# Optimization experiments

Measured on AMD Instinct MI355X. Metric: run time of the kernel, lower is better.

Reference implementation:

```python
import jax, jax.numpy as jnp
import numpy as np

EMBED_DIM = 1024
NUM_HEADS = 16
HEAD_DIM = EMBED_DIM // NUM_HEADS
B, S = 2, 2048


def setup_inputs() -> dict:
    key = jax.random.key(0)
    ks = jax.random.split(key, 10)
    inp = {
        "query": jax.random.normal(ks[0], (B, S, EMBED_DIM), dtype=jnp.float32),
        "key": jax.random.normal(ks[1], (B, S, EMBED_DIM), dtype=jnp.float32),
        "value": jax.random.normal(ks[2], (B, S, EMBED_DIM), dtype=jnp.float32),
        # 0 => masked key position (matches attn_mask == 0 in the torch code)
        "attn_mask": jax.random.randint(ks[3], (B, S), 0, 2, dtype=jnp.int32),
        "Wq": jax.random.normal(ks[4], (EMBED_DIM, EMBED_DIM), dtype=jnp.float32) * 0.02,
        "bq": jnp.zeros((EMBED_DIM,), dtype=jnp.float32),
        "Wk": jax.random.normal(ks[5], (EMBED_DIM, EMBED_DIM), dtype=jnp.float32) * 0.02,
        "bk": jnp.zeros((EMBED_DIM,), dtype=jnp.float32),
        "Wv": jax.random.normal(ks[6], (EMBED_DIM, EMBED_DIM), dtype=jnp.float32) * 0.02,
        "bv": jnp.zeros((EMBED_DIM,), dtype=jnp.float32),
    }
    return inp


def _proj_heads(x, W, b):
    # x: [B, S, E] -> [B, H, S, D]  (nn.Linear uses x @ W.T + b)
    y = x @ W.T + b
    Bx, Sx, E = y.shape
    return y.reshape(Bx, Sx, NUM_HEADS, HEAD_DIM).transpose(0, 2, 1, 3)


def reference(query, key, value, attn_mask, Wq, bq, Wk, bk, Wv, bv):
    q = _proj_heads(query, Wq, bq)   # [B,H,S,D]
    k = _proj_heads(key, Wk, bk)     # [B,H,S,D]
    v = _proj_heads(value, Wv, bv)   # [B,H,S,D]
    inv_scale = float(EMBED_DIM) ** 0.5  # NOTE: original divides by sqrt(embed_dim), not sqrt(head_dim)
    scores = jnp.einsum("bhqd,bhkd->bhqk", q, k) / inv_scale  # [B,H,S,S]
    mask = (attn_mask == 0)[:, None, None, :]  # [B,1,1,S] -> broadcast over [B,H,S,S]
    scores = jnp.where(mask, -jnp.inf, scores)
    attn = jax.nn.softmax(scores, axis=-1)
    # dropout omitted for deterministic reference (see notes)
    out = jnp.einsum("bhqk,bhkd->bhqd", attn, v)  # [B,H,S,D]
    return out
```

## Files before the change

### kernel.cpp

```cpp
#include <hip/hip_runtime.h>
#include <hip/hip_bf16.h>

constexpr int BB = 2;
constexpr int SS = 2048;
constexpr int EE = 1024;
constexpr int HH = 16;
constexpr int DD = 64;
constexpr int MM = BB * SS;
constexpr int CX = MM * EE;
constexpr int CW = EE * EE;
#define QSCALE 0.045084220027780106f

typedef __attribute__((ext_vector_type(8))) short short8;
typedef __attribute__((ext_vector_type(4))) float floatx4;
typedef __attribute__((ext_vector_type(4))) unsigned uintx4;

union fragu { uintx4 u; short8 s; };

__device__ inline short bf16bits(float x) {
    __hip_bfloat16 h = __float2bfloat16(x);
    return *reinterpret_cast<short*>(&h);
}

__device__ inline unsigned pkbf(float a, float b) {
    return (unsigned)(unsigned short)bf16bits(a) |
           ((unsigned)(unsigned short)bf16bits(b) << 16);
}

__device__ inline float fast_exp2(float x) {
#if __has_builtin(__builtin_amdgcn_exp2f)
    return __builtin_amdgcn_exp2f(x);
#else
    return exp2f(x);
#endif
}

__device__ inline void gl_lds16(const __hip_bfloat16* g, const short* l) {
    __builtin_amdgcn_global_load_lds(
        (const __attribute__((address_space(1))) void*)g,
        (__attribute__((address_space(3))) void*)l, 16, 0, 0);
}

__device__ inline int sigma_row(int p) {
    return (p & 0x23) | ((p & 0x0C) << 1) | ((p & 0x10) >> 2);
}

__global__ __launch_bounds__(256) void convert_kernel(
    const float* __restrict__ x0, const float* __restrict__ x1, const float* __restrict__ x2,
    const float* __restrict__ w0, const float* __restrict__ w1, const float* __restrict__ w2,
    __hip_bfloat16* __restrict__ xb, __hip_bfloat16* __restrict__ wb)
{
    const long long e = (long long)(blockIdx.x * 256 + threadIdx.x) * 8;
    const float* src;
    __hip_bfloat16* dst;
    if (e < 3LL * CX) {
        const int z = (int)(e >> 22);
        const int off = (int)(e & (CX - 1));
        src = ((z == 0) ? x0 : (z == 1) ? x1 : x2) + off;
        dst = xb + e;
    } else {
        const long long e2 = e - 3LL * CX;
        const int z = (int)(e2 >> 20);
        const int off = (int)(e2 & (CW - 1));
        src = ((z == 0) ? w0 : (z == 1) ? w1 : w2) + off;
        dst = wb + e2;
    }
    const float4 a = reinterpret_cast<const float4*>(src)[0];
    const float4 b = reinterpret_cast<const float4*>(src)[1];
    short8 r;
    r[0] = bf16bits(a.x); r[1] = bf16bits(a.y); r[2] = bf16bits(a.z); r[3] = bf16bits(a.w);
    r[4] = bf16bits(b.x); r[5] = bf16bits(b.y); r[6] = bf16bits(b.z); r[7] = bf16bits(b.w);
    *reinterpret_cast<short8*>(dst) = r;
}

__global__ __launch_bounds__(256) void proj_gemm(
    const __hip_bfloat16* __restrict__ xb,
    const __hip_bfloat16* __restrict__ wb,
    const float* __restrict__ bq, const float* __restrict__ bk, const float* __restrict__ bv,
    __hip_bfloat16* __restrict__ qws,
    __hip_bfloat16* __restrict__ kws,
    __hip_bfloat16* __restrict__ vtws)
{
    const int which = blockIdx.z;
    const __hip_bfloat16* A = xb + (size_t)which * CX;
    const __hip_bfloat16* W = wb + (size_t)which * CW;
    const float* bias = (which == 0) ? bq : (which == 1) ? bk : bv;

    const int m0   = blockIdx.x * 128;
    const int n0   = blockIdx.y * 128;
    const int tid  = threadIdx.x;
    const int wave = tid >> 6;
    const int lane = tid & 63;
    const int l15  = lane & 15;
    const int quad = lane >> 4;
    const int wr   = wave >> 1;
    const int wc   = wave & 1;

    __shared__ __align__(16) short As[128 * 32];
    __shared__ __align__(16) short Bs[128 * 32];

    const int dpos  = (lane & 7) ^ (lane >> 3);
    const int drloc = 2 * (lane >> 3) + (dpos >> 2);
    const int dgran = (dpos & 3) * 8;

    const int rbase = (l15 >> 1) * 64;
    const int rslot = (((l15 & 1) * 4 + quad) ^ (l15 >> 1)) * 8;

    floatx4 acc[4][4] = {};

    for (int k0 = 0; k0 < EE; k0 += 32) {
        __syncthreads();
        #pragma unroll
        for (int p = 0; p < 2; ++p) {
            const int rb16 = wave * 32 + p * 16;
            gl_lds16(A + (size_t)(m0 + rb16 + drloc) * EE + k0 + dgran, &As[rb16 * 32]);
            gl_lds16(W + (size_t)(n0 + rb16 + drloc) * EE + k0 + dgran, &Bs[rb16 * 32]);
        }
        __syncthreads();

        short8 af[4], bf[4];
        #pragma unroll
        for (int mt = 0; mt < 4; ++mt)
            af[mt] = *reinterpret_cast<const short8*>(
                &As[(wr * 32 + mt * 8) * 64 + rbase + rslot]);
        #pragma unroll
        for (int nt = 0; nt < 4; ++nt)
            bf[nt] = *reinterpret_cast<const short8*>(
                &Bs[(wc * 32 + nt * 8) * 64 + rbase + rslot]);

        #pragma unroll
        for (int mt = 0; mt < 4; ++mt)
            #pragma unroll
            for (int nt = 0; nt < 4; ++nt)
                acc[mt][nt] = __builtin_amdgcn_mfma_f32_16x16x32_bf16(af[mt], bf[nt], acc[mt][nt], 0, 0, 0);
    }

    #pragma unroll
    for (int nt = 0; nt < 4; ++nt) {
        const int n = n0 + wc * 64 + nt * 16 + l15;
        const float bval = bias[n];
        const int h = n >> 6, d = n & 63;
        #pragma unroll
        for (int mt = 0; mt < 4; ++mt) {
            #pragma unroll
            for (int r = 0; r < 4; ++r) {
                const int m = m0 + wr * 64 + mt * 16 + quad * 4 + r;
                const int b = m >> 11;
                const int s = m & (SS - 1);
                float val = acc[mt][nt][r] + bval;
                if (which == 0) val *= QSCALE;
                const __hip_bfloat16 hv = __float2bfloat16(val);
                if (which == 0)
                    qws[(((size_t)b * HH + h) * SS + s) * DD + d] = hv;
                else if (which == 1)
                    kws[(((size_t)b * HH + h) * SS + s) * DD + d] = hv;
                else
                    vtws[(((size_t)b * HH + h) * DD + d) * SS + s] = hv;
            }
        }
    }
}

__global__ __launch_bounds__(256) void attn_kernel(
    const __hip_bfloat16* __restrict__ qws,
    const __hip_bfloat16* __restrict__ kws,
    const __hip_bfloat16* __restrict__ vtws,
    const int* __restrict__ amask,
    float* __restrict__ out)
{
    const int flatb = blockIdx.y * gridDim.x + blockIdx.x;
    const int bh    = 4 * (flatb & 7) + ((flatb >> 3) & 3);
    const int b     = bh >> 4;
    const int q0    = (flatb >> 5) * 128;
    const int tid  = threadIdx.x;
    const int wave = tid >> 6;
    const int lane = tid & 63;
    const int l15  = lane & 15;
    const int quad = lane >> 4;

    const __hip_bfloat16* Q  = qws  + (size_t)bh * SS * DD;
    const __hip_bfloat16* K  = kws  + (size_t)bh * SS * DD;
    const __hip_bfloat16* VT = vtws + (size_t)bh * DD * SS;
    const int* msk = amask + b * SS;

    __shared__ __align__(16) short Ks[2][64 * 64];
    __shared__ __align__(16) short Vs[2][64 * 64];
    __shared__ __align__(16) float Ms[SS];

    #pragma unroll
    for (int i = 0; i < 2; ++i) {
        const int j = tid + i * 256;
        const int4 m4 = reinterpret_cast<const int4*>(msk)[j];
        float4 f4;
        f4.x = (float)m4.x; f4.y = (float)m4.y; f4.z = (float)m4.z; f4.w = (float)m4.w;
        reinterpret_cast<float4*>(Ms)[j] = f4;
    }

    const int qrow = q0 + wave * 32 + l15;
    const short8 qa0 = *reinterpret_cast<const short8*>(Q + (size_t)qrow * DD + quad * 8);
    const short8 qa1 = *reinterpret_cast<const short8*>(Q + (size_t)qrow * DD + 32 + quad * 8);
    const short8 qa2 = *reinterpret_cast<const short8*>(Q + (size_t)(qrow + 16) * DD + quad * 8);
    const short8 qa3 = *reinterpret_cast<const short8*>(Q + (size_t)(qrow + 16) * DD + 32 + quad * 8);

    const int swz = l15 & 7;

    const int srow = lane >> 3;
    const int sg   = ((lane & 7) ^ srow) * 8;
    const int sk0  = sigma_row(wave * 16 + srow);
    const int sk1  = sigma_row(wave * 16 + 8 + srow);

    float l0 = 0.f, l1 = 0.f;
    floatx4 acc0[4] = {}, acc1[4] = {};

    {
        const int rb0 = wave * 16, rb1 = rb0 + 8;
        gl_lds16(K + (size_t)sk0 * DD + sg, &Ks[0][rb0 * 64]);
        gl_lds16(VT + (size_t)(rb0 + srow) * SS + sg, &Vs[0][rb0 * 64]);
        gl_lds16(K + (size_t)sk1 * DD + sg, &Ks[0][rb1 * 64]);
        gl_lds16(VT + (size_t)(rb1 + srow) * SS + sg, &Vs[0][rb1 * 64]);
    }
    __asm__ volatile("s_waitcnt vmcnt(0) lgkmcnt(0)" ::: "memory");
    __builtin_amdgcn_s_barrier();

    for (int t = 0; t < SS / 64; ++t) {
        const int cur = t & 1;

        if (t + 1 < SS / 64) {
            const int kn = (t + 1) * 64;
            const int rb0 = wave * 16, rb1 = rb0 + 8;
            gl_lds16(K + (size_t)(kn + sk0) * DD + sg, &Ks[cur ^ 1][rb0 * 64]);
            gl_lds16(VT + (size_t)(rb0 + srow) * SS + kn + sg, &Vs[cur ^ 1][rb0 * 64]);
            gl_lds16(K + (size_t)(kn + sk1) * DD + sg, &Ks[cur ^ 1][rb1 * 64]);
            gl_lds16(VT + (size_t)(rb1 + srow) * SS + kn + sg, &Vs[cur ^ 1][rb1 * 64]);
        }
        const int kt = t * 64;

        floatx4 s0[4], s1[4];
        __builtin_amdgcn_s_setprio(1);
        #pragma unroll
        for (int f = 0; f < 4; ++f) {
            const int krow = (f * 16 + l15) * 64;
            const short8 ka = *reinterpret_cast<const short8*>(&Ks[cur][krow + (quad ^ swz) * 8]);
            const short8 kb = *reinterpret_cast<const short8*>(&Ks[cur][krow + ((quad + 4) ^ swz) * 8]);
            floatx4 z = {};
            z = __builtin_amdgcn_mfma_f32_16x16x32_bf16(ka, qa0, z, 0, 0, 0);
            z = __builtin_amdgcn_mfma_f32_16x16x32_bf16(kb, qa1, z, 0, 0, 0);
            s0[f] = z;
            floatx4 w = {};
            w = __builtin_amdgcn_mfma_f32_16x16x32_bf16(ka, qa2, w, 0, 0, 0);
            w = __builtin_amdgcn_mfma_f32_16x16x32_bf16(kb, qa3, w, 0, 0, 0);
            s1[f] = w;
        }
        __builtin_amdgcn_s_setprio(0);

        fragu fa0, fa1, fb0, fb1;
        #pragma unroll
        for (int f = 0; f < 4; ++f) {
            const float4 mf = *reinterpret_cast<const float4*>(
                &Ms[kt + 32 * (f >> 1) + 8 * quad + 4 * (f & 1)]);
            const float e00 = fast_exp2(s0[f][0]) * mf.x;
            const float e01 = fast_exp2(s0[f][1]) * mf.y;
            const float e02 = fast_exp2(s0[f][2]) * mf.z;
            const float e03 = fast_exp2(s0[f][3]) * mf.w;
            const float e10 = fast_exp2(s1[f][0]) * mf.x;
            const float e11 = fast_exp2(s1[f][1]) * mf.y;
            const float e12 = fast_exp2(s1[f][2]) * mf.z;
            const float e13 = fast_exp2(s1[f][3]) * mf.w;
            l0 += e00 + e01 + e02 + e03;
            l1 += e10 + e11 + e12 + e13;
            uintx4& da = (f < 2) ? fa0.u : fa1.u;
            uintx4& db = (f < 2) ? fb0.u : fb1.u;
            const int i0 = (f & 1) * 2;
            da[i0]     = pkbf(e00, e01);
            da[i0 + 1] = pkbf(e02, e03);
            db[i0]     = pkbf(e10, e11);
            db[i0 + 1] = pkbf(e12, e13);
        }

        __builtin_amdgcn_s_setprio(1);
        #pragma unroll
        for (int nt = 0; nt < 4; ++nt) {
            const int vrow = (nt * 16 + l15) * 64;
            const short8 vb0 = *reinterpret_cast<const short8*>(&Vs[cur][vrow + (quad ^ swz) * 8]);
            const short8 vb1 = *reinterpret_cast<const short8*>(&Vs[cur][vrow + ((quad + 4) ^ swz) * 8]);
            acc0[nt] = __builtin_amdgcn_mfma_f32_16x16x32_bf16(fa0.s, vb0, acc0[nt], 0, 0, 0);
            acc0[nt] = __builtin_amdgcn_mfma_f32_16x16x32_bf16(fa1.s, vb1, acc0[nt], 0, 0, 0);
            acc1[nt] = __builtin_amdgcn_mfma_f32_16x16x32_bf16(fb0.s, vb0, acc1[nt], 0, 0, 0);
            acc1[nt] = __builtin_amdgcn_mfma_f32_16x16x32_bf16(fb1.s, vb1, acc1[nt], 0, 0, 0);
        }
        __builtin_amdgcn_s_setprio(0);

        if (t + 1 < SS / 64) {
            __asm__ volatile("s_waitcnt vmcnt(0)" ::: "memory");
            __builtin_amdgcn_s_barrier();
        }
    }

    l0 += __shfl_xor(l0, 16, 64); l0 += __shfl_xor(l0, 32, 64);
    l1 += __shfl_xor(l1, 16, 64); l1 += __shfl_xor(l1, 32, 64);
    float i0[4], i1[4];
    #pragma unroll
    for (int r = 0; r < 4; ++r) {
        i0[r] = 1.f / __shfl(l0, quad * 4 + r, 16);
        i1[r] = 1.f / __shfl(l1, quad * 4 + r, 16);
    }

    const size_t obase = (size_t)bh * SS * DD;
    #pragma unroll
    for (int nt = 0; nt < 4; ++nt)
        #pragma unroll
        for (int r = 0; r < 4; ++r) {
            const int qq = q0 + wave * 32 + quad * 4 + r;
            const int d  = nt * 16 + l15;
            out[obase + (size_t)qq * DD + d] = acc0[nt][r] * i0[r];
            out[obase + (size_t)(qq + 16) * DD + d] = acc1[nt][r] * i1[r];
        }
}

extern "C" void kernel_launch(void* const* d_in, const int* in_sizes, int n_in,
                              void* d_out, int out_size, void* d_ws, size_t ws_size,
                              hipStream_t stream) {
    const float* q    = (const float*)d_in[0];
    const float* k    = (const float*)d_in[1];
    const float* v    = (const float*)d_in[2];
    const int*   mask = (const int*)d_in[3];
    const float* Wq   = (const float*)d_in[4];
    const float* bq   = (const float*)d_in[5];
    const float* Wk   = (const float*)d_in[6];
    const float* bk   = (const float*)d_in[7];
    const float* Wv   = (const float*)d_in[8];
    const float* bv   = (const float*)d_in[9];
    float* out = (float*)d_out;

    __hip_bfloat16* qws  = (__hip_bfloat16*)d_ws;
    __hip_bfloat16* kws  = qws + (size_t)CX;
    __hip_bfloat16* vtws = kws + (size_t)CX;
    __hip_bfloat16* xb   = vtws + (size_t)CX;
    __hip_bfloat16* wb   = xb + (size_t)3 * CX;

    const int cvt_blocks = (3 * CX + 3 * CW) / (256 * 8);
    convert_kernel<<<dim3(cvt_blocks), 256, 0, stream>>>(q, k, v, Wq, Wk, Wv, xb, wb);
    proj_gemm<<<dim3(MM / 128, EE / 128, 3), 256, 0, stream>>>(
        xb, wb, bq, bk, bv, qws, kws, vtws);
    attn_kernel<<<dim3(SS / 128, BB * HH), 256, 0, stream>>>(
        qws, kws, vtws, mask, out);
}
```

Measured before the change: 203.1 us.

## Triple-buffer GEMM and attention tiles; compute softmax row sums with MFMA

Both the projection GEMM and the attention kernel move from single or double LDS buffering to a three-stage ring, prefetching two tiles ahead and waiting with partial vmcnt so loads overlap compute with one barrier per step. The GEMM also raises wave priority around its MFMA block. In attention, the per-lane scalar accumulation of softmax denominators and the final shuffle reduction are replaced by extra MFMAs against a ones vector, which sum the bf16-rounded probabilities on the matrix cores. This costs more LDS per block, which may lower occupancy. It also means the denominator now sums the bf16-rounded values rather than the fp32 ones.

```diff
diff --git a/kernel.cpp b/kernel.cpp
--- a/kernel.cpp
+++ b/kernel.cpp
@@ -96,8 +96,8 @@
     const int wr   = wave >> 1;
     const int wc   = wave & 1;
 
-    __shared__ __align__(16) short As[128 * 32];
-    __shared__ __align__(16) short Bs[128 * 32];
+    __shared__ __align__(16) short As[3][128 * 32];
+    __shared__ __align__(16) short Bs[3][128 * 32];
 
     const int dpos  = (lane & 7) ^ (lane >> 3);
     const int drloc = 2 * (lane >> 3) + (dpos >> 2);
@@ -108,31 +108,58 @@
 
     floatx4 acc[4][4] = {};
 
-    for (int k0 = 0; k0 < EE; k0 += 32) {
-        __syncthreads();
+    constexpr int NK = EE / 32;
+
+    #pragma unroll
+    for (int tt = 0; tt < 2; ++tt) {
+        const int k0 = tt * 32;
         #pragma unroll
         for (int p = 0; p < 2; ++p) {
             const int rb16 = wave * 32 + p * 16;
-            gl_lds16(A + (size_t)(m0 + rb16 + drloc) * EE + k0 + dgran, &As[rb16 * 32]);
-            gl_lds16(W + (size_t)(n0 + rb16 + drloc) * EE + k0 + dgran, &Bs[rb16 * 32]);
-        }
-        __syncthreads();
+            gl_lds16(A + (size_t)(m0 + rb16 + drloc) * EE + k0 + dgran, &As[tt][rb16 * 32]);
+            gl_lds16(W + (size_t)(n0 + rb16 + drloc) * EE + k0 + dgran, &Bs[tt][rb16 * 32]);
+        }
+    }
+    __asm__ volatile("s_waitcnt vmcnt(4) lgkmcnt(0)" ::: "memory");
+    __builtin_amdgcn_s_barrier();
+
+    for (int t = 0; t < NK; ++t) {
+        const int cur = t % 3;
+
+        if (t + 2 < NK) {
+            const int nxt = (t + 2) % 3;
+            const int k0 = (t + 2) * 32;
+            #pragma unroll
+            for (int p = 0; p < 2; ++p) {
+                const int rb16 = wave * 32 + p * 16;
+                gl_lds16(A + (size_t)(m0 + rb16 + drloc) * EE + k0 + dgran, &As[nxt][rb16 * 32]);
+                gl_lds16(W + (size_t)(n0 + rb16 + drloc) * EE + k0 + dgran, &Bs[nxt][rb16 * 32]);
+            }
+        }
 
         short8 af[4], bf[4];
         #pragma unroll
         for (int mt = 0; mt < 4; ++mt)
             af[mt] = *reinterpret_cast<const short8*>(
-                &As[(wr * 32 + mt * 8) * 64 + rbase + rslot]);
+                &As[cur][(wr * 32 + mt * 8) * 64 + rbase + rslot]);
         #pragma unroll
         for (int nt = 0; nt < 4; ++nt)
             bf[nt] = *reinterpret_cast<const short8*>(
-                &Bs[(wc * 32 + nt * 8) * 64 + rbase + rslot]);
-
+                &Bs[cur][(wc * 32 + nt * 8) * 64 + rbase + rslot]);
+
+        __builtin_amdgcn_s_setprio(1);
         #pragma unroll
         for (int mt = 0; mt < 4; ++mt)
             #pragma unroll
             for (int nt = 0; nt < 4; ++nt)
                 acc[mt][nt] = __builtin_amdgcn_mfma_f32_16x16x32_bf16(af[mt], bf[nt], acc[mt][nt], 0, 0, 0);
+        __builtin_amdgcn_s_setprio(0);
+
+        if (t + 1 < NK) {
+            if (t + 2 < NK) { __asm__ volatile("s_waitcnt vmcnt(4)" ::: "memory"); }
+            else            { __asm__ volatile("s_waitcnt vmcnt(0)" ::: "memory"); }
+            __builtin_amdgcn_s_barrier();
+        }
     }
 
     #pragma unroll
@@ -183,8 +210,8 @@
     const __hip_bfloat16* VT = vtws + (size_t)bh * DD * SS;
     const int* msk = amask + b * SS;
 
-    __shared__ __align__(16) short Ks[2][64 * 64];
-    __shared__ __align__(16) short Vs[2][64 * 64];
+    __shared__ __align__(16) short Ks[3][64 * 64];
+    __shared__ __align__(16) short Vs[3][64 * 64];
     __shared__ __align__(16) float Ms[SS];
 
     #pragma unroll
@@ -204,34 +231,42 @@
 
     const int swz = l15 & 7;
 
+    short8 ones;
+    #pragma unroll
+    for (int i = 0; i < 8; ++i) ones[i] = (short)0x3F80;
+
     const int srow = lane >> 3;
     const int sg   = ((lane & 7) ^ srow) * 8;
     const int sk0  = sigma_row(wave * 16 + srow);
     const int sk1  = sigma_row(wave * 16 + 8 + srow);
-
-    float l0 = 0.f, l1 = 0.f;
+    const int rb0  = wave * 16, rb1 = rb0 + 8;
+
     floatx4 acc0[4] = {}, acc1[4] = {};
-
-    {
-        const int rb0 = wave * 16, rb1 = rb0 + 8;
-        gl_lds16(K + (size_t)sk0 * DD + sg, &Ks[0][rb0 * 64]);
-        gl_lds16(VT + (size_t)(rb0 + srow) * SS + sg, &Vs[0][rb0 * 64]);
-        gl_lds16(K + (size_t)sk1 * DD + sg, &Ks[0][rb1 * 64]);
-        gl_lds16(VT + (size_t)(rb1 + srow) * SS + sg, &Vs[0][rb1 * 64]);
-    }
-    __asm__ volatile("s_waitcnt vmcnt(0) lgkmcnt(0)" ::: "memory");
+    floatx4 accl0 = {}, accl1 = {};
+
+    constexpr int NT = SS / 64;
+
+    #pragma unroll
+    for (int tt = 0; tt < 2; ++tt) {
+        const int kn = tt * 64;
+        gl_lds16(K + (size_t)(kn + sk0) * DD + sg, &Ks[tt][rb0 * 64]);
+        gl_lds16(VT + (size_t)(rb0 + srow) * SS + kn + sg, &Vs[tt][rb0 * 64]);
+        gl_lds16(K + (size_t)(kn + sk1) * DD + sg, &Ks[tt][rb1 * 64]);
+        gl_lds16(VT + (size_t)(rb1 + srow) * SS + kn + sg, &Vs[tt][rb1 * 64]);
+    }
+    __asm__ volatile("s_waitcnt vmcnt(4) lgkmcnt(0)" ::: "memory");
     __builtin_amdgcn_s_barrier();
 
-    for (int t = 0; t < SS / 64; ++t) {
-        const int cur = t & 1;
-
-        if (t + 1 < SS / 64) {
-            const int kn = (t + 1) * 64;
-            const int rb0 = wave * 16, rb1 = rb0 + 8;
-            gl_lds16(K + (size_t)(kn + sk0) * DD + sg, &Ks[cur ^ 1][rb0 * 64]);
-            gl_lds16(VT + (size_t)(rb0 + srow) * SS + kn + sg, &Vs[cur ^ 1][rb0 * 64]);
-            gl_lds16(K + (size_t)(kn + sk1) * DD + sg, &Ks[cur ^ 1][rb1 * 64]);
-            gl_lds16(VT + (size_t)(rb1 + srow) * SS + kn + sg, &Vs[cur ^ 1][rb1 * 64]);
+    for (int t = 0; t < NT; ++t) {
+        const int cur = t % 3;
+
+        if (t + 2 < NT) {
+            const int nxt = (t + 2) % 3;
+            const int kn = (t + 2) * 64;
+            gl_lds16(K + (size_t)(kn + sk0) * DD + sg, &Ks[nxt][rb0 * 64]);
+            gl_lds16(VT + (size_t)(rb0 + srow) * SS + kn + sg, &Vs[nxt][rb0 * 64]);
+            gl_lds16(K + (size_t)(kn + sk1) * DD + sg, &Ks[nxt][rb1 * 64]);
+            gl_lds16(VT + (size_t)(rb1 + srow) * SS + kn + sg, &Vs[nxt][rb1 * 64]);
         }
         const int kt = t * 64;
 
@@ -266,8 +301,6 @@
             const float e11 = fast_exp2(s1[f][1]) * mf.y;
             const float e12 = fast_exp2(s1[f][2]) * mf.z;
             const float e13 = fast_exp2(s1[f][3]) * mf.w;
-            l0 += e00 + e01 + e02 + e03;
-            l1 += e10 + e11 + e12 + e13;
             uintx4& da = (f < 2) ? fa0.u : fa1.u;
             uintx4& db = (f < 2) ? fb0.u : fb1.u;
             const int i0 = (f & 1) * 2;
@@ -278,6 +311,10 @@
         }
 
         __builtin_amdgcn_s_setprio(1);
+        accl0 = __builtin_amdgcn_mfma_f32_16x16x32_bf16(fa0.s, ones, accl0, 0, 0, 0);
+        accl0 = __builtin_amdgcn_mfma_f32_16x16x32_bf16(fa1.s, ones, accl0, 0, 0, 0);
+        accl1 = __builtin_amdgcn_mfma_f32_16x16x32_bf16(fb0.s, ones, accl1, 0, 0, 0);
+        accl1 = __builtin_amdgcn_mfma_f32_16x16x32_bf16(fb1.s, ones, accl1, 0, 0, 0);
         #pragma unroll
         for (int nt = 0; nt < 4; ++nt) {
             const int vrow = (nt * 16 + l15) * 64;
@@ -290,19 +327,18 @@
         }
         __builtin_amdgcn_s_setprio(0);
 
-        if (t + 1 < SS / 64) {
-            __asm__ volatile("s_waitcnt vmcnt(0)" ::: "memory");
+        if (t + 1 < NT) {
+            if (t + 2 < NT) { __asm__ volatile("s_waitcnt vmcnt(4)" ::: "memory"); }
+            else            { __asm__ volatile("s_waitcnt vmcnt(0)" ::: "memory"); }
             __builtin_amdgcn_s_barrier();
         }
     }
 
-    l0 += __shfl_xor(l0, 16, 64); l0 += __shfl_xor(l0, 32, 64);
-    l1 += __shfl_xor(l1, 16, 64); l1 += __shfl_xor(l1, 32, 64);
     float i0[4], i1[4];
     #pragma unroll
     for (int r = 0; r < 4; ++r) {
-        i0[r] = 1.f / __shfl(l0, quad * 4 + r, 16);
-        i1[r] = 1.f / __shfl(l1, quad * 4 + r, 16);
+        i0[r] = 1.f / accl0[r];
+        i1[r] = 1.f / accl1[r];
     }
 
     const size_t obase = (size_t)bh * SS * DD;
```

New measurement: 202.4 us. Within noise of the previous version (-0.3%).

## Deepen LDS prefetch pipelines in projection and attention, sum softmax denominators via MFMA

Applied to the files above, without the earlier changes.

The projection GEMM moves from a single LDS buffer with two barriers per k-step to a triple-buffered ring that prefetches two steps ahead, with one barrier per step that waits only on the older loads (vmcnt(4)). The attention kernel moves from double to quadruple K/V buffering with a two-tile lookahead and partial vmcnt waits, so global loads overlap more compute. It also replaces the per-lane scalar row-sum and shuffle reduction of softmax denominators with MFMAs against a vector of bf16 ones. These changes are meant to hide load latency and cut VALU work, at the cost of more LDS per block (possible occupancy loss) and denominators summed from bf16-rounded probabilities.

```diff
diff --git a/kernel.cpp b/kernel.cpp
--- a/kernel.cpp
+++ b/kernel.cpp
@@ -44,6 +44,9 @@
 __device__ inline int sigma_row(int p) {
     return (p & 0x23) | ((p & 0x0C) << 1) | ((p & 0x10) >> 2);
 }
+
+#define TURN4 { __asm__ volatile("s_waitcnt vmcnt(4)" ::: "memory"); __builtin_amdgcn_s_barrier(); }
+#define TURN0 { __asm__ volatile("s_waitcnt vmcnt(0)" ::: "memory"); __builtin_amdgcn_s_barrier(); }
 
 __global__ __launch_bounds__(256) void convert_kernel(
     const float* __restrict__ x0, const float* __restrict__ x1, const float* __restrict__ x2,
@@ -73,6 +76,33 @@
     *reinterpret_cast<short8*>(dst) = r;
 }
 
+#define PROJ_PF(NXT, T2) { \
+    const int k0 = (T2) * 32; \
+    _Pragma("unroll") \
+    for (int p = 0; p < 2; ++p) { \
+        const int rb16 = wave * 32 + p * 16; \
+        gl_lds16(A + (size_t)(m0 + rb16 + drloc) * EE + k0 + dgran, &As[NXT][rb16 * 32]); \
+        gl_lds16(W + (size_t)(n0 + rb16 + drloc) * EE + k0 + dgran, &Bs[NXT][rb16 * 32]); \
+    } }
+
+#define PROJ_BODY(CUR) { \
+    short8 af[4], bf[4]; \
+    _Pragma("unroll") \
+    for (int mt = 0; mt < 4; ++mt) \
+        af[mt] = *reinterpret_cast<const short8*>( \
+            &As[CUR][(wr * 32 + mt * 8) * 64 + rbase + rslot]); \
+    _Pragma("unroll") \
+    for (int nt = 0; nt < 4; ++nt) \
+        bf[nt] = *reinterpret_cast<const short8*>( \
+            &Bs[CUR][(wc * 32 + nt * 8) * 64 + rbase + rslot]); \
+    __builtin_amdgcn_s_setprio(1); \
+    _Pragma("unroll") \
+    for (int mt = 0; mt < 4; ++mt) \
+        _Pragma("unroll") \
+        for (int nt = 0; nt < 4; ++nt) \
+            acc[mt][nt] = __builtin_amdgcn_mfma_f32_16x16x32_bf16(af[mt], bf[nt], acc[mt][nt], 0, 0, 0); \
+    __builtin_amdgcn_s_setprio(0); }
+
 __global__ __launch_bounds__(256) void proj_gemm(
     const __hip_bfloat16* __restrict__ xb,
     const __hip_bfloat16* __restrict__ wb,
@@ -96,8 +126,8 @@
     const int wr   = wave >> 1;
     const int wc   = wave & 1;
 
-    __shared__ __align__(16) short As[128 * 32];
-    __shared__ __align__(16) short Bs[128 * 32];
+    __shared__ __align__(16) short As[3][128 * 32];
+    __shared__ __align__(16) short Bs[3][128 * 32];
 
     const int dpos  = (lane & 7) ^ (lane >> 3);
     const int drloc = 2 * (lane >> 3) + (dpos >> 2);
@@ -108,32 +138,18 @@
 
     floatx4 acc[4][4] = {};
 
-    for (int k0 = 0; k0 < EE; k0 += 32) {
-        __syncthreads();
-        #pragma unroll
-        for (int p = 0; p < 2; ++p) {
-            const int rb16 = wave * 32 + p * 16;
-            gl_lds16(A + (size_t)(m0 + rb16 + drloc) * EE + k0 + dgran, &As[rb16 * 32]);
-            gl_lds16(W + (size_t)(n0 + rb16 + drloc) * EE + k0 + dgran, &Bs[rb16 * 32]);
-        }
-        __syncthreads();
-
-        short8 af[4], bf[4];
-        #pragma unroll
-        for (int mt = 0; mt < 4; ++mt)
-            af[mt] = *reinterpret_cast<const short8*>(
-                &As[(wr * 32 + mt * 8) * 64 + rbase + rslot]);
-        #pragma unroll
-        for (int nt = 0; nt < 4; ++nt)
-            bf[nt] = *reinterpret_cast<const short8*>(
-                &Bs[(wc * 32 + nt * 8) * 64 + rbase + rslot]);
-
-        #pragma unroll
-        for (int mt = 0; mt < 4; ++mt)
-            #pragma unroll
-            for (int nt = 0; nt < 4; ++nt)
-                acc[mt][nt] = __builtin_amdgcn_mfma_f32_16x16x32_bf16(af[mt], bf[nt], acc[mt][nt], 0, 0, 0);
-    }
+    PROJ_PF(0, 0);
+    PROJ_PF(1, 1);
+    __asm__ volatile("s_waitcnt vmcnt(4)" ::: "memory");
+    __builtin_amdgcn_s_barrier();
+
+    for (int t = 0; t < 30; t += 3) {
+        PROJ_PF(2, t + 2); PROJ_BODY(0); TURN4;
+        PROJ_PF(0, t + 3); PROJ_BODY(1); TURN4;
+        PROJ_PF(1, t + 4); PROJ_BODY(2); TURN4;
+    }
+    PROJ_BODY(0); TURN0;
+    PROJ_BODY(1);
 
     #pragma unroll
     for (int nt = 0; nt < 4; ++nt) {
@@ -161,6 +177,70 @@
     }
 }
 
+#define ATTN_PF(NXT, T2) { \
+    const int kn = (T2) * 64; \
+    gl_lds16(K + (size_t)(kn + sk0) * DD + sg, &Ks[NXT][rb0 * 64]); \
+    gl_lds16(VT + (size_t)(rb0 + srow) * SS + kn + sg, &Vs[NXT][rb0 * 64]); \
+    gl_lds16(K + (size_t)(kn + sk1) * DD + sg, &Ks[NXT][rb1 * 64]); \
+    gl_lds16(VT + (size_t)(rb1 + srow) * SS + kn + sg, &Vs[NXT][rb1 * 64]); }
+
+#define ATTN_BODY(CUR, T) { \
+    const int kt = (T) * 64; \
+    floatx4 s0[4], s1[4]; \
+    __builtin_amdgcn_s_setprio(1); \
+    _Pragma("unroll") \
+    for (int f = 0; f < 4; ++f) { \
+        const int krow = (f * 16 + l15) * 64; \
+        const short8 ka = *reinterpret_cast<const short8*>(&Ks[CUR][krow + (quad ^ swz) * 8]); \
+        const short8 kb = *reinterpret_cast<const short8*>(&Ks[CUR][krow + ((quad + 4) ^ swz) * 8]); \
+        floatx4 z = {}; \
+        z = __builtin_amdgcn_mfma_f32_16x16x32_bf16(ka, qa0, z, 0, 0, 0); \
+        z = __builtin_amdgcn_mfma_f32_16x16x32_bf16(kb, qa1, z, 0, 0, 0); \
+        s0[f] = z; \
+        floatx4 w = {}; \
+        w = __builtin_amdgcn_mfma_f32_16x16x32_bf16(ka, qa2, w, 0, 0, 0); \
+        w = __builtin_amdgcn_mfma_f32_16x16x32_bf16(kb, qa3, w, 0, 0, 0); \
+        s1[f] = w; \
+    } \
+    __builtin_amdgcn_s_setprio(0); \
+    fragu fa0, fa1, fb0, fb1; \
+    _Pragma("unroll") \
+    for (int f = 0; f < 4; ++f) { \
+        const float4 mf = *reinterpret_cast<const float4*>( \
+            &Ms[kt + 32 * (f >> 1) + 8 * quad + 4 * (f & 1)]); \
+        const float e00 = fast_exp2(s0[f][0]) * mf.x; \
+        const float e01 = fast_exp2(s0[f][1]) * mf.y; \
+        const float e02 = fast_exp2(s0[f][2]) * mf.z; \
+        const float e03 = fast_exp2(s0[f][3]) * mf.w; \
+        const float e10 = fast_exp2(s1[f][0]) * mf.x; \
+        const float e11 = fast_exp2(s1[f][1]) * mf.y; \
+        const float e12 = fast_exp2(s1[f][2]) * mf.z; \
+        const float e13 = fast_exp2(s1[f][3]) * mf.w; \
+        uintx4& da = (f < 2) ? fa0.u : fa1.u; \
+        uintx4& db = (f < 2) ? fb0.u : fb1.u; \
+        const int i0 = (f & 1) * 2; \
+        da[i0]     = pkbf(e00, e01); \
+        da[i0 + 1] = pkbf(e02, e03); \
+        db[i0]     = pkbf(e10, e11); \
+        db[i0 + 1] = pkbf(e12, e13); \
+    } \
+    __builtin_amdgcn_s_setprio(1); \
+    accl0 = __builtin_amdgcn_mfma_f32_16x16x32_bf16(fa0.s, ones, accl0, 0, 0, 0); \
+    accl0 = __builtin_amdgcn_mfma_f32_16x16x32_bf16(fa1.s, ones, accl0, 0, 0, 0); \
+    accl1 = __builtin_amdgcn_mfma_f32_16x16x32_bf16(fb0.s, ones, accl1, 0, 0, 0); \
+    accl1 = __builtin_amdgcn_mfma_f32_16x16x32_bf16(fb1.s, ones, accl1, 0, 0, 0); \
+    _Pragma("unroll") \
+    for (int nt = 0; nt < 4; ++nt) { \
+        const int vrow = (nt * 16 + l15) * 64; \
+        const short8 vb0 = *reinterpret_cast<const short8*>(&Vs[CUR][vrow + (quad ^ swz) * 8]); \
+        const short8 vb1 = *reinterpret_cast<const short8*>(&Vs[CUR][vrow + ((quad + 4) ^ swz) * 8]); \
+        acc0[nt] = __builtin_amdgcn_mfma_f32_16x16x32_bf16(fa0.s, vb0, acc0[nt], 0, 0, 0); \
+        acc0[nt] = __builtin_amdgcn_mfma_f32_16x16x32_bf16(fa1.s, vb1, acc0[nt], 0, 0, 0); \
+        acc1[nt] = __builtin_amdgcn_mfma_f32_16x16x32_bf16(fb0.s, vb0, acc1[nt], 0, 0, 0); \
+        acc1[nt] = __builtin_amdgcn_mfma_f32_16x16x32_bf16(fb1.s, vb1, acc1[nt], 0, 0, 0); \
+    } \
+    __builtin_amdgcn_s_setprio(0); }
+
 __global__ __launch_bounds__(256) void attn_kernel(
     const __hip_bfloat16* __restrict__ qws,
     const __hip_bfloat16* __restrict__ kws,
@@ -183,8 +263,8 @@
     const __hip_bfloat16* VT = vtws + (size_t)bh * DD * SS;
     const int* msk = amask + b * SS;
 
-    __shared__ __align__(16) short Ks[2][64 * 64];
-    __shared__ __align__(16) short Vs[2][64 * 64];
+    __shared__ __align__(16) short Ks[4][64 * 64];
+    __shared__ __align__(16) short Vs[4][64 * 64];
     __shared__ __align__(16) float Ms[SS];
 
     #pragma unroll
@@ -204,105 +284,40 @@
 
     const int swz = l15 & 7;
 
+    short8 ones;
+    #pragma unroll
+    for (int i = 0; i < 8; ++i) ones[i] = (short)0x3F80;
+
     const int srow = lane >> 3;
     const int sg   = ((lane & 7) ^ srow) * 8;
     const int sk0  = sigma_row(wave * 16 + srow);
     const int sk1  = sigma_row(wave * 16 + 8 + srow);
-
-    float l0 = 0.f, l1 = 0.f;
+    const int rb0  = wave * 16, rb1 = rb0 + 8;
+
     floatx4 acc0[4] = {}, acc1[4] = {};
-
-    {
-        const int rb0 = wave * 16, rb1 = rb0 + 8;
-        gl_lds16(K + (size_t)sk0 * DD + sg, &Ks[0][rb0 * 64]);
-        gl_lds16(VT + (size_t)(rb0 + srow) * SS + sg, &Vs[0][rb0 * 64]);
-        gl_lds16(K + (size_t)sk1 * DD + sg, &Ks[0][rb1 * 64]);
-        gl_lds16(VT + (size_t)(rb1 + srow) * SS + sg, &Vs[0][rb1 * 64]);
-    }
-    __asm__ volatile("s_waitcnt vmcnt(0) lgkmcnt(0)" ::: "memory");
+    floatx4 accl0 = {}, accl1 = {};
+
+    ATTN_PF(0, 0);
+    ATTN_PF(1, 1);
+    __asm__ volatile("s_waitcnt vmcnt(4) lgkmcnt(0)" ::: "memory");
     __builtin_amdgcn_s_barrier();
 
-    for (int t = 0; t < SS / 64; ++t) {
-        const int cur = t & 1;
-
-        if (t + 1 < SS / 64) {
-            const int kn = (t + 1) * 64;
-            const int rb0 = wave * 16, rb1 = rb0 + 8;
-            gl_lds16(K + (size_t)(kn + sk0) * DD + sg, &Ks[cur ^ 1][rb0 * 64]);
-            gl_lds16(VT + (size_t)(rb0 + srow) * SS + kn + sg, &Vs[cur ^ 1][rb0 * 64]);
-            gl_lds16(K + (size_t)(kn + sk1) * DD + sg, &Ks[cur ^ 1][rb1 * 64]);
-            gl_lds16(VT + (size_t)(rb1 + srow) * SS + kn + sg, &Vs[cur ^ 1][rb1 * 64]);
-        }
-        const int kt = t * 64;
-
-        floatx4 s0[4], s1[4];
-        __builtin_amdgcn_s_setprio(1);
-        #pragma unroll
-        for (int f = 0; f < 4; ++f) {
-            const int krow = (f * 16 + l15) * 64;
-            const short8 ka = *reinterpret_cast<const short8*>(&Ks[cur][krow + (quad ^ swz) * 8]);
-            const short8 kb = *reinterpret_cast<const short8*>(&Ks[cur][krow + ((quad + 4) ^ swz) * 8]);
-            floatx4 z = {};
-            z = __builtin_amdgcn_mfma_f32_16x16x32_bf16(ka, qa0, z, 0, 0, 0);
-            z = __builtin_amdgcn_mfma_f32_16x16x32_bf16(kb, qa1, z, 0, 0, 0);
-            s0[f] = z;
-            floatx4 w = {};
-            w = __builtin_amdgcn_mfma_f32_16x16x32_bf16(ka, qa2, w, 0, 0, 0);
-            w = __builtin_amdgcn_mfma_f32_16x16x32_bf16(kb, qa3, w, 0, 0, 0);
-            s1[f] = w;
-        }
-        __builtin_amdgcn_s_setprio(0);
-
-        fragu fa0, fa1, fb0, fb1;
-        #pragma unroll
-        for (int f = 0; f < 4; ++f) {
-            const float4 mf = *reinterpret_cast<const float4*>(
-                &Ms[kt + 32 * (f >> 1) + 8 * quad + 4 * (f & 1)]);
-            const float e00 = fast_exp2(s0[f][0]) * mf.x;
-            const float e01 = fast_exp2(s0[f][1]) * mf.y;
-            const float e02 = fast_exp2(s0[f][2]) * mf.z;
-            const float e03 = fast_exp2(s0[f][3]) * mf.w;
-            const float e10 = fast_exp2(s1[f][0]) * mf.x;
-            const float e11 = fast_exp2(s1[f][1]) * mf.y;
-            const float e12 = fast_exp2(s1[f][2]) * mf.z;
-            const float e13 = fast_exp2(s1[f][3]) * mf.w;
-            l0 += e00 + e01 + e02 + e03;
-            l1 += e10 + e11 + e12 + e13;
-            uintx4& da = (f < 2) ? fa0.u : fa1.u;
-            uintx4& db = (f < 2) ? fb0.u : fb1.u;
-            const int i0 = (f & 1) * 2;
-            da[i0]     = pkbf(e00, e01);
-            da[i0 + 1] = pkbf(e02, e03);
-            db[i0]     = pkbf(e10, e11);
-            db[i0 + 1] = pkbf(e12, e13);
-        }
-
-        __builtin_amdgcn_s_setprio(1);
-        #pragma unroll
-        for (int nt = 0; nt < 4; ++nt) {
-            const int vrow = (nt * 16 + l15) * 64;
-            const short8 vb0 = *reinterpret_cast<const short8*>(&Vs[cur][vrow + (quad ^ swz) * 8]);
-            const short8 vb1 = *reinterpret_cast<const short8*>(&Vs[cur][vrow + ((quad + 4) ^ swz) * 8]);
-            acc0[nt] = __builtin_amdgcn_mfma_f32_16x16x32_bf16(fa0.s, vb0, acc0[nt], 0, 0, 0);
-            acc0[nt] = __builtin_amdgcn_mfma_f32_16x16x32_bf16(fa1.s, vb1, acc0[nt], 0, 0, 0);
-            acc1[nt] = __builtin_amdgcn_mfma_f32_16x16x32_bf16(fb0.s, vb0, acc1[nt], 0, 0, 0);
-            acc1[nt] = __builtin_amdgcn_mfma_f32_16x16x32_bf16(fb1.s, vb1, acc1[nt], 0, 0, 0);
-        }
-        __builtin_amdgcn_s_setprio(0);
-
-        if (t + 1 < SS / 64) {
-            __asm__ volatile("s_waitcnt vmcnt(0)" ::: "memory");
-            __builtin_amdgcn_s_barrier();
-        }
-    }
-
-    l0 += __shfl_xor(l0, 16, 64); l0 += __shfl_xor(l0, 32, 64);
-    l1 += __shfl_xor(l1, 16, 64); l1 += __shfl_xor(l1, 32, 64);
+    for (int t = 0; t < 28; t += 4) {
+        ATTN_PF(2, t + 2); ATTN_BODY(0, t);     TURN4;
+        ATTN_PF(3, t + 3); ATTN_BODY(1, t + 1); TURN4;
+        ATTN_PF(0, t + 4); ATTN_BODY(2, t + 2); TURN4;
+        ATTN_PF(1, t + 5); ATTN_BODY(3, t + 3); TURN4;
+    }
+    ATTN_PF(2, 30); ATTN_BODY(0, 28); TURN4;
+    ATTN_PF(3, 31); ATTN_BODY(1, 29); TURN4;
+    ATTN_BODY(2, 30); TURN0;
+    ATTN_BODY(3, 31);
+
     float i0[4], i1[4];
     #pragma unroll
     for (int r = 0; r < 4; ++r) {
-        i0[r] = 1.f / __shfl(l0, quad * 4 + r, 16);
-        i1[r] = 1.f / __shfl(l1, quad * 4 + r, 16);
+        i0[r] = 1.f / accl0[r];
+        i1[r] = 1.f / accl1[r];
     }
 
     const size_t obase = (size_t)bh * SS * DD;
```

Result: slower. 212.6 us (+4.7%).
